# Optimization experiments

Hardware: AMD Instinct MI355X
Metric: run time of the kernel (lower is better)

Reference implementation:

```python
import jax, jax.numpy as jnp
import numpy as np

N_NODES = 100000
N_EDGES = 1600000
NFEAT = 128
NHID = 128
NS = 64
NCLASS = 16
B = 8192


def setup_inputs() -> dict:
    key = jax.random.key(0)
    ks = jax.random.split(key, 12)
    s = jax.random.normal(ks[0], (B, NS), dtype=jnp.float32)
    x = jax.random.normal(ks[1], (N_NODES, NFEAT), dtype=jnp.float32)
    row = jax.random.randint(ks[2], (N_EDGES,), 0, N_NODES)
    col = jax.random.randint(ks[3], (N_EDGES,), 0, N_NODES)
    val = jax.random.uniform(ks[4], (N_EDGES,), dtype=jnp.float32)
    index = jax.random.randint(ks[5], (B,), 0, N_NODES)
    # learned parameters (glorot-ish scale)
    W1 = jax.random.normal(ks[6], (NFEAT, NHID), dtype=jnp.float32) / np.sqrt(NFEAT)
    b1 = jnp.zeros((NHID,), dtype=jnp.float32)
    W2 = jax.random.normal(ks[7], (NHID, NHID), dtype=jnp.float32) / np.sqrt(NHID)
    b2 = jnp.zeros((NHID,), dtype=jnp.float32)
    Wl = jax.random.normal(ks[8], (NHID + NS, NCLASS), dtype=jnp.float32) / np.sqrt(NHID + NS)
    bl = jnp.zeros((NCLASS,), dtype=jnp.float32)
    return {"s": s, "x": x, "row": row, "col": col, "val": val,
            "index": index, "W1": W1, "b1": b1, "W2": W2, "b2": b2,
            "Wl": Wl, "bl": bl}


def reference(s, x, row, col, val, index, W1, b1, W2, b2, Wl, bl):
    n = x.shape[0]

    def spmm(h):
        # adj @ h with adj in COO form: out[r] += val_e * h[c]
        return jax.ops.segment_sum(val[:, None] * h[col], row, num_segments=n)

    # dropout is identity in eval mode (training=False)
    h = jax.nn.relu(spmm(x @ W1) + b1)          # gc1 + relu
    h = spmm(h @ W2) + b2                        # gc2
    z = jnp.concatenate([h[index], s], axis=1) @ Wl + bl  # [B, nclass]
    return jax.nn.log_softmax(z, axis=1)
```

## Files before the change

### kernel.cpp

```cpp
#include <hip/hip_runtime.h>
#include <hip/hip_fp16.h>
#include <math.h>

#define N_NODES 100000
#define N_EDGES 1600000
#define NFEAT 128
#define NHID 128
#define NS 64
#define NCLASS 16
#define BB 8192

#define B1_SHIFT 11
#define NB1 49
#define SUB_SHIFT 5
#define NSUB 3125
#define CHUNKA 2048
#define HWG 256
#define BINC_CAP 2048

#define NSLICE 8
#define SLICEF 16

typedef unsigned long long ull;
typedef unsigned int uint;


__device__ __forceinline__ unsigned short f2bf(float f) {
  unsigned int u = __float_as_uint(f);
  return (unsigned short)((u + 0x7fffu + ((u >> 16) & 1u)) >> 16);
}
__device__ __forceinline__ unsigned int packbf2(float lo, float hi) {
  return (unsigned int)f2bf(lo) | ((unsigned int)f2bf(hi) << 16);
}


__device__ __forceinline__ __half2 h2zero() {
  return __builtin_bit_cast(__half2, 0u);
}
__device__ __forceinline__ __half2 h2shfl_add(__half2 a, int m) {
  int t = __shfl_xor(__builtin_bit_cast(int, a), m);
  return __hadd2(a, __builtin_bit_cast(__half2, t));
}
__device__ __forceinline__ uint relu2(uint u) {
  uint mm = ((u >> 15) & 0x10001u) * 0xFFFFu;
  return u & ~mm;
}
union U4H { uint4 u4; __half2 h[4]; };

__device__ __forceinline__ void fma_row_h(__half2* acc, __half2 v, uint4 u) {
  U4H q; q.u4 = u;
#pragma unroll
  for (int k = 0; k < 4; ++k) acc[k] = __hfma2(v, q.h[k], acc[k]);
}
__device__ __forceinline__ __half2 edge_vh2(uint e) {
  uint hb = e >> 17;
  return __builtin_bit_cast(__half2, hb * 0x10001u);
}


__device__ __forceinline__ ull pack_edge(float v, int r, int c) {
  return ((ull)(__float_as_uint(v) >> 2) << 34) | ((ull)(unsigned)r << 17) | (unsigned)c;
}
__device__ __forceinline__ int edge_col(ull p) { return (int)(p & 0x1FFFFu); }
__device__ __forceinline__ int edge_row(ull p) { return (int)((unsigned)(p >> 17) & 0x1FFFFu); }
__device__ __forceinline__ float edge_val(ull p) {
  return __uint_as_float(((unsigned)(p >> 34)) << 2);
}
__device__ __forceinline__ uint pack4(ull p) {
  uint hb = (uint)__half_as_ushort(__float2half(edge_val(p)));
  return (uint)edge_col(p) | (hb << 17);
}
__device__ __forceinline__ int keep_test(const uint* keep, int r) {
  return (keep[r >> 5] >> (r & 31)) & 1u;
}


__global__ __launch_bounds__(256) void selbuild_kernel(const int* __restrict__ index,
                                                       int* __restrict__ sel,
                                                       uint* __restrict__ keep) {
  int t = blockIdx.x * 256 + threadIdx.x;
  int r = index[t];
  sel[r] = 1;
  atomicOr(&keep[r >> 5], 1u << (r & 31));
}

__global__ __launch_bounds__(256) void selflag_kernel(const int* __restrict__ row,
                                                      const int* __restrict__ col,
                                                      const int* __restrict__ sel,
                                                      uint* __restrict__ keep) {
  int i = blockIdx.x * blockDim.x + threadIdx.x;
  int stride = gridDim.x * blockDim.x;
  for (; i < N_EDGES; i += stride)
    if (sel[row[i]]) {
      int c = col[i];
      atomicOr(&keep[c >> 5], 1u << (c & 31));
    }
}


__global__ __launch_bounds__(256) void rowlist_kernel(const uint* __restrict__ keep,
                                                      int* __restrict__ rowlist,
                                                      int* __restrict__ nkept) {
  int w = blockIdx.x * 256 + threadIdx.x;
  if (w >= NSUB) return;
  uint b = keep[w];
  int c = __popc(b);
  if (!c) return;
  int base = atomicAdd(nkept, c);
  int r0 = w << 5;
  while (b) {
    int i = __ffs(b) - 1;
    rowlist[base++] = r0 + i;
    b &= b - 1;
  }
}


__global__ __launch_bounds__(256) void histsub_kernel(const int* __restrict__ row,
                                                      const uint* __restrict__ keep,
                                                      int* __restrict__ subcnt) {
  __shared__ int lh[NSUB];
  int tid = threadIdx.x;
  for (int i = tid; i < NSUB; i += 256) lh[i] = 0;
  __syncthreads();
  for (long i = (long)blockIdx.x * 256 + tid; i < N_EDGES; i += (long)HWG * 256) {
    int r = row[i];
    if (keep_test(keep, r)) atomicAdd(&lh[r >> SUB_SHIFT], 1);
  }
  __syncthreads();
  for (int i = tid; i < NSUB; i += 256) {
    int c = lh[i];
    if (c) atomicAdd(&subcnt[i], c);
  }
}


__global__ __launch_bounds__(1024) void scanall_kernel(const int* __restrict__ subcnt,
                                                       int* __restrict__ sub_offs,
                                                       int* __restrict__ gcur1,
                                                       int* __restrict__ gcur2) {
  __shared__ int sd[1024];
  int tid = threadIdx.x;
  int b0 = tid * 4;
  int vv[4];
  int loc = 0;
#pragma unroll
  for (int k = 0; k < 4; ++k) {
    int i = b0 + k;
    vv[k] = (i < NSUB) ? subcnt[i] : 0;
    loc += vv[k];
  }
  sd[tid] = loc;
  __syncthreads();
  for (int o = 1; o < 1024; o <<= 1) {
    int add = (tid >= o) ? sd[tid - o] : 0;
    __syncthreads();
    sd[tid] += add;
    __syncthreads();
  }
  int pre = sd[tid] - loc;
#pragma unroll
  for (int k = 0; k < 4; ++k) {
    int i = b0 + k;
    if (i < NSUB) {
      sub_offs[i] = pre;
      gcur2[i] = pre;
      if ((i & 63) == 0) gcur1[i >> 6] = pre;
      pre += vv[k];
    }
  }
  if (tid == 1023) sub_offs[NSUB] = sd[1023];
}


__global__ __launch_bounds__(256) void binA_kernel(const int* __restrict__ row,
                                                   const int* __restrict__ col,
                                                   const float* __restrict__ val,
                                                   const uint* __restrict__ keep,
                                                   int* __restrict__ gcur1,
                                                   ull* __restrict__ ebuf1) {
  __shared__ ull stage[CHUNKA];
  __shared__ short bkt[CHUNKA];
  __shared__ int hist[NB1], lofs[NB1 + 1], lcur[NB1], gbase[NB1];
  int tid = threadIdx.x;
  for (long base = (long)blockIdx.x * CHUNKA; base < N_EDGES; base += (long)gridDim.x * CHUNKA) {
    int cnt = (int)min((long)CHUNKA, (long)N_EDGES - base);
    if (tid < NB1) hist[tid] = 0;
    __syncthreads();
    ull e[8]; int bk[8];
#pragma unroll
    for (int v = 0; v < 8; ++v) {
      int i = v * 256 + tid;
      bk[v] = -1;
      if (i < cnt) {
        long g = base + i;
        int r = row[g];
        if (keep_test(keep, r)) {
          e[v] = pack_edge(val[g], r, col[g]);
          bk[v] = r >> B1_SHIFT;
          atomicAdd(&hist[bk[v]], 1);
        }
      }
    }
    __syncthreads();
    if (tid < 64) {
      int h = (tid < NB1) ? hist[tid] : 0;
      int x = h;
      for (int o = 1; o < 64; o <<= 1) {
        int y = __shfl_up(x, o);
        if (tid >= o) x += y;
      }
      if (tid < NB1) { lofs[tid] = x - h; lcur[tid] = x - h; }
      if (tid == 63) lofs[NB1] = x;
    }
    __syncthreads();
#pragma unroll
    for (int v = 0; v < 8; ++v) {
      if (bk[v] >= 0) {
        int pos = atomicAdd(&lcur[bk[v]], 1);
        stage[pos] = e[v];
        bkt[pos] = (short)bk[v];
      }
    }
    __syncthreads();
    if (tid < NB1) {
      int h = hist[tid];
      if (h > 0) gbase[tid] = atomicAdd(&gcur1[tid], h);
    }
    __syncthreads();
    int tot = lofs[NB1];
    for (int s = tid; s < tot; s += 256) {
      int lo = bkt[s];
      ebuf1[gbase[lo] + (s - lofs[lo])] = stage[s];
    }
    __syncthreads();
  }
}


__global__ __launch_bounds__(256) void binB_kernel(const ull* __restrict__ ebuf1,
                                                   const int* __restrict__ sub_offs,
                                                   int* __restrict__ gcur2,
                                                   ull* __restrict__ edat8) {
  __shared__ ull stage[CHUNKA];
  __shared__ short bkt[CHUNKA];
  __shared__ int hist[64], lofs[65], lcur[64], gbase[64];
  int tid = threadIdx.x;
  int b1 = blockIdx.x >> 3, w = blockIdx.x & 7;
  int rbeg = sub_offs[b1 << 6];
  int rend = sub_offs[min((b1 + 1) << 6, NSUB)];
  for (int base = rbeg + w * CHUNKA; base < rend; base += 8 * CHUNKA) {
    int cnt = min(CHUNKA, rend - base);
    if (tid < 64) hist[tid] = 0;
    __syncthreads();
    ull e[8]; int bk[8];
#pragma unroll
    for (int v = 0; v < 8; ++v) {
      int i = v * 256 + tid;
      bk[v] = -1;
      if (i < cnt) {
        e[v] = ebuf1[base + i];
        bk[v] = (edge_row(e[v]) >> SUB_SHIFT) - (b1 << 6);
        atomicAdd(&hist[bk[v]], 1);
      }
    }
    __syncthreads();
    if (tid < 64) {
      int h = hist[tid];
      int x = h;
      for (int o = 1; o < 64; o <<= 1) {
        int y = __shfl_up(x, o);
        if (tid >= o) x += y;
      }
      lofs[tid] = x - h;
      lcur[tid] = x - h;
      if (tid == 63) lofs[64] = x;
    }
    __syncthreads();
#pragma unroll
    for (int v = 0; v < 8; ++v) {
      if (bk[v] >= 0) {
        int pos = atomicAdd(&lcur[bk[v]], 1);
        stage[pos] = e[v];
        bkt[pos] = (short)bk[v];
      }
    }
    __syncthreads();
    if (tid < 64) {
      int h = hist[tid];
      if (h > 0) gbase[tid] = atomicAdd(&gcur2[(b1 << 6) + tid], h);
    }
    __syncthreads();
    for (int s = tid; s < cnt; s += 256) {
      int lo = bkt[s];
      edat8[gbase[lo] + (s - lofs[lo])] = stage[s];
    }
    __syncthreads();
  }
}


__global__ __launch_bounds__(256) void binC_kernel(const int* __restrict__ sub_offs,
                                                   const ull* __restrict__ edat8,
                                                   ull* __restrict__ ebuf1,
                                                   uint* __restrict__ edat4,
                                                   int* __restrict__ offs) {
  __shared__ ull es[BINC_CAP];
  __shared__ int rcnt[32], rcur[32];
  int s = blockIdx.x, tid = threadIdx.x;
  int r0 = s << SUB_SHIFT;
  int beg = sub_offs[s], end = sub_offs[s + 1];
  int n = end - beg;
  if (tid < 32) rcnt[tid] = 0;
  __syncthreads();
  if (n <= BINC_CAP) {
    for (int i = tid; i < n; i += 256) {
      ull p = edat8[beg + i];
      es[i] = p;
      atomicAdd(&rcnt[edge_row(p) & 31], 1);
    }
    __syncthreads();
    if (tid < 32) {
      int h = rcnt[tid];
      int x = h;
      for (int o = 1; o < 32; o <<= 1) {
        int y = __shfl_up(x, o, 32);
        if (tid >= o) x += y;
      }
      rcur[tid] = x - h;
      offs[r0 + tid] = beg + x - h;
      if (s == NSUB - 1 && tid == 31) offs[N_NODES] = end;
    }
    __syncthreads();
    for (int i = tid; i < n; i += 256) {
      ull p = es[i];
      int pos = atomicAdd(&rcur[edge_row(p) & 31], 1);
      edat4[beg + pos] = pack4(p);
    }
  } else {
    for (int i = tid; i < n; i += 256) {
      ull p = edat8[beg + i];
      ebuf1[beg + i] = p;
      atomicAdd(&rcnt[edge_row(p) & 31], 1);
    }
    __syncthreads();
    if (tid < 32) {
      int h = rcnt[tid];
      int x = h;
      for (int o = 1; o < 32; o <<= 1) {
        int y = __shfl_up(x, o, 32);
        if (tid >= o) x += y;
      }
      rcur[tid] = x - h;
      offs[r0 + tid] = beg + x - h;
      if (s == NSUB - 1 && tid == 31) offs[N_NODES] = end;
    }
    __syncthreads();
    for (int i = tid; i < n; i += 256) {
      ull p = ebuf1[beg + i];
      int pos = atomicAdd(&rcur[edge_row(p) & 31], 1);
      edat4[beg + pos] = pack4(p);
    }
  }
}


typedef __attribute__((ext_vector_type(8))) __bf16 bf16x8;
typedef __attribute__((ext_vector_type(4))) float f32x4;
union FragU { uint4 u; bf16x8 b; };

#define LDSTR 68

__global__ __launch_bounds__(256) void gemm1_kernel(const float* __restrict__ A,
                                                    const float* __restrict__ W,
                                                    unsigned short* __restrict__ C,
                                                    int nrows) {
  __shared__ uint As_s[64 * LDSTR];
  __shared__ uint Wt_s[128 * LDSTR];
  int tid = threadIdx.x;
  int rbase = blockIdx.x * 64;

  {
    int n = tid & 127, hh = tid >> 7;
#pragma unroll
    for (int kk = 0; kk < 32; ++kk) {
      int kc = hh * 32 + kk;
      Wt_s[n * LDSTR + kc] = packbf2(W[(2 * kc) * 128 + n], W[(2 * kc + 1) * 128 + n]);
    }
  }
  {
    const float4* src = (const float4*)(A + (long)rbase * 128);
#pragma unroll
    for (int i = 0; i < 8; ++i) {
      int f = i * 256 + tid;
      int m = f >> 5;
      float4 v = (rbase + m < nrows) ? src[f] : make_float4(0.f, 0.f, 0.f, 0.f);
      int c = (f & 31) * 2;
      As_s[m * LDSTR + c]     = packbf2(v.x, v.y);
      As_s[m * LDSTR + c + 1] = packbf2(v.z, v.w);
    }
  }
  __syncthreads();

  int w = tid >> 6, lane = tid & 63;
  int quad = lane >> 4, lr = lane & 15;
  int n0 = w * 32;

  f32x4 acc[4][2];
#pragma unroll
  for (int mt = 0; mt < 4; ++mt)
#pragma unroll
    for (int nt = 0; nt < 2; ++nt) acc[mt][nt] = (f32x4){0.f, 0.f, 0.f, 0.f};

#pragma unroll
  for (int kk = 0; kk < 4; ++kk) {
    int kc = kk * 16 + quad * 4;
    FragU fb0, fb1;
    fb0.u = *(const uint4*)&Wt_s[(n0 + lr) * LDSTR + kc];
    fb1.u = *(const uint4*)&Wt_s[(n0 + 16 + lr) * LDSTR + kc];
#pragma unroll
    for (int mt = 0; mt < 4; ++mt) {
      FragU fa;
      fa.u = *(const uint4*)&As_s[(mt * 16 + lr) * LDSTR + kc];
      acc[mt][0] = __builtin_amdgcn_mfma_f32_16x16x32_bf16(fa.b, fb0.b, acc[mt][0], 0, 0, 0);
      acc[mt][1] = __builtin_amdgcn_mfma_f32_16x16x32_bf16(fa.b, fb1.b, acc[mt][1], 0, 0, 0);
    }
  }

#pragma unroll
  for (int mt = 0; mt < 4; ++mt) {
#pragma unroll
    for (int nt = 0; nt < 2; ++nt) {
      __half* cs = (__half*)(C + (size_t)(w * 2 + nt) * (N_NODES * SLICEF));
#pragma unroll
      for (int r = 0; r < 4; ++r) {
        int row = rbase + mt * 16 + quad * 4 + r;
        if (row < nrows) cs[(size_t)row * SLICEF + lr] = __float2half(acc[mt][nt][r]);
      }
    }
  }
}


__global__ __launch_bounds__(256) void gemm2f_kernel(const float* __restrict__ g2,
                                                     const float* __restrict__ W2,
                                                     const float* __restrict__ b2,
                                                     const float* __restrict__ s_in,
                                                     const float* __restrict__ Wl,
                                                     const float* __restrict__ bl,
                                                     float* __restrict__ out) {
  __shared__ uint smem[13056];
  uint* Wt_s = smem;
  uint* As_s = smem + 128 * LDSTR;
  float* ts  = (float*)smem;
  float* Wls = (float*)(smem + 128 * LDSTR);
  int tid = threadIdx.x;
  int rbase = blockIdx.x * 64;

  {
    int n = tid & 127, hh = tid >> 7;
#pragma unroll
    for (int kk = 0; kk < 32; ++kk) {
      int kc = hh * 32 + kk;
      Wt_s[n * LDSTR + kc] = packbf2(W2[(2 * kc) * 128 + n], W2[(2 * kc + 1) * 128 + n]);
    }
  }
  {
    const float4* src = (const float4*)(g2 + (long)rbase * 128);
#pragma unroll
    for (int i = 0; i < 8; ++i) {
      int f = i * 256 + tid;
      int m = f >> 5, c = (f & 31) * 2;
      float4 v = src[f];
      As_s[m * LDSTR + c]     = packbf2(v.x, v.y);
      As_s[m * LDSTR + c + 1] = packbf2(v.z, v.w);
    }
  }
  __syncthreads();

  int w = tid >> 6, lane = tid & 63;
  int quad = lane >> 4, lr = lane & 15;
  int n0 = w * 32;

  f32x4 acc[4][2];
#pragma unroll
  for (int mt = 0; mt < 4; ++mt)
#pragma unroll
    for (int nt = 0; nt < 2; ++nt) acc[mt][nt] = (f32x4){0.f, 0.f, 0.f, 0.f};

#pragma unroll
  for (int kk = 0; kk < 4; ++kk) {
    int kc = kk * 16 + quad * 4;
    FragU fb0, fb1;
    fb0.u = *(const uint4*)&Wt_s[(n0 + lr) * LDSTR + kc];
    fb1.u = *(const uint4*)&Wt_s[(n0 + 16 + lr) * LDSTR + kc];
#pragma unroll
    for (int mt = 0; mt < 4; ++mt) {
      FragU fa;
      fa.u = *(const uint4*)&As_s[(mt * 16 + lr) * LDSTR + kc];
      acc[mt][0] = __builtin_amdgcn_mfma_f32_16x16x32_bf16(fa.b, fb0.b, acc[mt][0], 0, 0, 0);
      acc[mt][1] = __builtin_amdgcn_mfma_f32_16x16x32_bf16(fa.b, fb1.b, acc[mt][1], 0, 0, 0);
    }
  }
  __syncthreads();

#pragma unroll
  for (int mt = 0; mt < 4; ++mt) {
#pragma unroll
    for (int nt = 0; nt < 2; ++nt) {
      int col = n0 + nt * 16 + lr;
      float bv = b2[col];
#pragma unroll
      for (int r = 0; r < 4; ++r)
        ts[(mt * 16 + quad * 4 + r) * 129 + col] = acc[mt][nt][r] + bv;
    }
  }
  for (int i = tid; i < 192 * 16; i += 256) Wls[i] = Wl[i];
  __syncthreads();

  int q = lane & 3;
  int mrow = w * 16 + (lane >> 2);
  int b = rbase + mrow;
  float z[16];
#pragma unroll
  for (int c = 0; c < 16; ++c) z[c] = 0.f;
  int k0 = q * 48;
  for (int kk = 0; kk < 48; ++kk) {
    int k = k0 + kk;
    float xv = (k < 128) ? ts[mrow * 129 + k] : s_in[(long)b * 64 + (k - 128)];
    const float* wp = Wls + k * 16;
#pragma unroll
    for (int c = 0; c < 16; ++c) z[c] = fmaf(xv, wp[c], z[c]);
  }
#pragma unroll
  for (int c = 0; c < 16; ++c) {
    z[c] += __shfl_xor(z[c], 1);
    z[c] += __shfl_xor(z[c], 2);
  }
  if (q == 0) {
#pragma unroll
    for (int c = 0; c < 16; ++c) z[c] += bl[c];
    float mx = z[0];
#pragma unroll
    for (int c = 1; c < 16; ++c) mx = fmaxf(mx, z[c]);
    float sum = 0.f;
#pragma unroll
    for (int c = 0; c < 16; ++c) sum += expf(z[c] - mx);
    float lse = mx + logf(sum);
    float4* ob = (float4*)(out + (long)b * 16);
    ob[0] = make_float4(z[0] - lse, z[1] - lse, z[2] - lse, z[3] - lse);
    ob[1] = make_float4(z[4] - lse, z[5] - lse, z[6] - lse, z[7] - lse);
    ob[2] = make_float4(z[8] - lse, z[9] - lse, z[10] - lse, z[11] - lse);
    ob[3] = make_float4(z[12] - lse, z[13] - lse, z[14] - lse, z[15] - lse);
  }
}


__global__ __launch_bounds__(256) void spmm_row_kernel(const int* __restrict__ offs,
                                                       const uint* __restrict__ edat4,
                                                       const unsigned short* __restrict__ a,
                                                       const float* __restrict__ bias,
                                                       unsigned short* __restrict__ h1,
                                                       const int* __restrict__ rowlist,
                                                       const int* __restrict__ nkept) {
  int nk = *nkept;
  int rblk = blockIdx.x >> 3;
  if (rblk * 32 >= nk) return;
  int s = blockIdx.x & 7;
  int tid = threadIdx.x, lane = tid & 63;
  int li = rblk * 32 + (tid >> 3);
  int g = (lane >> 1) & 3, h = lane & 1, h8 = h * 8;
  const unsigned short* as = a + (size_t)s * (N_NODES * SLICEF);
  bool active = li < nk;
  int r = 0, j = 0, jend = 0;
  if (active) {
    r = __builtin_nontemporal_load(&rowlist[li]);
    j = __builtin_nontemporal_load(&offs[r]) + g;
    jend = __builtin_nontemporal_load(&offs[r + 1]);
  }
  __half2 acc[4] = {h2zero(), h2zero(), h2zero(), h2zero()};
  for (; j + 4 < jend; j += 8) {
    uint e0 = __builtin_nontemporal_load(&edat4[j]);
    uint e1 = __builtin_nontemporal_load(&edat4[j + 4]);
    uint4 u0 = *(const uint4*)(as + (size_t)(e0 & 0x1FFFFu) * SLICEF + h8);
    uint4 u1 = *(const uint4*)(as + (size_t)(e1 & 0x1FFFFu) * SLICEF + h8);
    fma_row_h(acc, edge_vh2(e0), u0);
    fma_row_h(acc, edge_vh2(e1), u1);
  }
  if (j < jend) {
    uint e = __builtin_nontemporal_load(&edat4[j]);
    uint4 u = *(const uint4*)(as + (size_t)(e & 0x1FFFFu) * SLICEF + h8);
    fma_row_h(acc, edge_vh2(e), u);
  }
#pragma unroll
  for (int k = 0; k < 4; ++k) {
    acc[k] = h2shfl_add(acc[k], 2);
    acc[k] = h2shfl_add(acc[k], 4);
  }
  if (active && (lane & 6) == 0) {
    const float* bp = bias + s * SLICEF + h8;
    float4 b0 = *(const float4*)bp;
    float4 b1v = *(const float4*)(bp + 4);
    uint4 o;
    o.x = relu2(__builtin_bit_cast(uint, __hadd2(acc[0], __floats2half2_rn(b0.x, b0.y))));
    o.y = relu2(__builtin_bit_cast(uint, __hadd2(acc[1], __floats2half2_rn(b0.z, b0.w))));
    o.z = relu2(__builtin_bit_cast(uint, __hadd2(acc[2], __floats2half2_rn(b1v.x, b1v.y))));
    o.w = relu2(__builtin_bit_cast(uint, __hadd2(acc[3], __floats2half2_rn(b1v.z, b1v.w))));
    *(uint4*)(h1 + (size_t)s * (N_NODES * SLICEF) + (size_t)r * SLICEF + h8) = o;
  }
}

__global__ __launch_bounds__(256) void spmm_sel_kernel(const int* __restrict__ offs,
                                                       const uint* __restrict__ edat4,
                                                       const unsigned short* __restrict__ h1,
                                                       const int* __restrict__ index,
                                                       float* __restrict__ g2) {
  int s = blockIdx.x & 7;
  int bblk = blockIdx.x >> 3;
  int tid = threadIdx.x, lane = tid & 63;
  int b = bblk * 32 + (tid >> 3);
  int g = (lane >> 1) & 3, h = lane & 1, h8 = h * 8;
  const unsigned short* hs = h1 + (size_t)s * (N_NODES * SLICEF);
  int r = __builtin_nontemporal_load(&index[b]);
  int j = __builtin_nontemporal_load(&offs[r]) + g;
  int jend = __builtin_nontemporal_load(&offs[r + 1]);
  __half2 acc[4] = {h2zero(), h2zero(), h2zero(), h2zero()};
  for (; j + 4 < jend; j += 8) {
    uint e0 = __builtin_nontemporal_load(&edat4[j]);
    uint e1 = __builtin_nontemporal_load(&edat4[j + 4]);
    uint4 u0 = *(const uint4*)(hs + (size_t)(e0 & 0x1FFFFu) * SLICEF + h8);
    uint4 u1 = *(const uint4*)(hs + (size_t)(e1 & 0x1FFFFu) * SLICEF + h8);
    fma_row_h(acc, edge_vh2(e0), u0);
    fma_row_h(acc, edge_vh2(e1), u1);
  }
  if (j < jend) {
    uint e = __builtin_nontemporal_load(&edat4[j]);
    uint4 u = *(const uint4*)(hs + (size_t)(e & 0x1FFFFu) * SLICEF + h8);
    fma_row_h(acc, edge_vh2(e), u);
  }
#pragma unroll
  for (int k = 0; k < 4; ++k) {
    acc[k] = h2shfl_add(acc[k], 2);
    acc[k] = h2shfl_add(acc[k], 4);
  }
  if ((lane & 6) == 0) {
    float* op = g2 + (size_t)b * 128 + s * SLICEF + h8;
    *(float4*)op = make_float4(__low2float(acc[0]), __high2float(acc[0]),
                               __low2float(acc[1]), __high2float(acc[1]));
    *(float4*)(op + 4) = make_float4(__low2float(acc[2]), __high2float(acc[2]),
                                     __low2float(acc[3]), __high2float(acc[3]));
  }
}


extern "C" void kernel_launch(void* const* d_in, const int* in_sizes, int n_in,
                              void* d_out, int out_size, void* d_ws, size_t ws_size,
                              hipStream_t stream) {
  const float* s_in  = (const float*)d_in[0];
  const float* x     = (const float*)d_in[1];
  const int*   row   = (const int*)d_in[2];
  const int*   col   = (const int*)d_in[3];
  const float* val   = (const float*)d_in[4];
  const int*   index = (const int*)d_in[5];
  const float* W1    = (const float*)d_in[6];
  const float* b1    = (const float*)d_in[7];
  const float* W2    = (const float*)d_in[8];
  const float* b2    = (const float*)d_in[9];
  const float* Wl    = (const float*)d_in[10];
  const float* bl    = (const float*)d_in[11];
  float* out = (float*)d_out;

  ull* edat8 = (ull*)d_ws;
  ull* ebuf1 = edat8 + N_EDGES;
  uint* edat4 = (uint*)ebuf1;
  unsigned short* a  = (unsigned short*)(ebuf1 + N_EDGES);
  unsigned short* h1 = a + (size_t)N_NODES * 128;
  float* g2   = (float*)(h1 + (size_t)N_NODES * 128);
  int* sel    = (int*)(g2 + (size_t)BB * 128);
  int* rowlist = sel;
  int* subcnt = sel + N_NODES;
  uint* keep  = (uint*)(subcnt + NSUB);
  int* offs   = (int*)(keep + NSUB);
  int* sub_offs = offs + (N_NODES + 1);
  int* gcur1  = sub_offs + (NSUB + 1);
  int* gcur2  = gcur1 + NB1;
  int* nkept  = gcur2 + NSUB;

  hipMemsetAsync(sel, 0, (N_NODES + 2 * NSUB) * sizeof(int), stream);
  hipMemsetAsync(nkept, 0, sizeof(int), stream);

  selbuild_kernel<<<BB / 256, 256, 0, stream>>>(index, sel, keep);
  selflag_kernel<<<4096, 256, 0, stream>>>(row, col, sel, keep);
  histsub_kernel<<<HWG, 256, 0, stream>>>(row, keep, subcnt);
  scanall_kernel<<<1, 1024, 0, stream>>>(subcnt, sub_offs, gcur1, gcur2);
  rowlist_kernel<<<(NSUB + 255) / 256, 256, 0, stream>>>(keep, rowlist, nkept);

  binA_kernel<<<512, 256, 0, stream>>>(row, col, val, keep, gcur1, ebuf1);
  binB_kernel<<<NB1 * 8, 256, 0, stream>>>(ebuf1, sub_offs, gcur2, edat8);
  binC_kernel<<<NSUB, 256, 0, stream>>>(sub_offs, edat8, ebuf1, edat4, offs);

  gemm1_kernel<<<(N_NODES + 63) / 64, 256, 0, stream>>>(x, W1, a, N_NODES);
  spmm_row_kernel<<<NSUB * NSLICE, 256, 0, stream>>>(offs, edat4, a, b1, h1, rowlist, nkept);
  spmm_sel_kernel<<<(BB / 32) * NSLICE, 256, 0, stream>>>(offs, edat4, h1, index, g2);
  gemm2f_kernel<<<BB / 64, 256, 0, stream>>>(g2, W2, b2, s_in, Wl, bl, out);
}
```

Baseline: 357.9 us.

## Switch feature matrices from sliced layout to row-major with wave-per-row SpMM

Replaces the 8-slice column-partitioned layout of the intermediate feature matrices with plain row-major 128-wide rows. Each SpMM wave now handles one whole row (16 lanes by 8 features, 4 edge groups) and skips rows by testing the keep bitmap directly. This removes the rowlist compaction kernel and its memset, and the repeated per-slice reads of edge data. gemm1 now processes two 64-row tiles per block so the W1 staging is shared. The cost is launching a block for every node, including rows that are not kept, and reading edge lists through a single wave per row.

```diff
diff --git a/kernel.cpp b/kernel.cpp
--- a/kernel.cpp
+++ b/kernel.cpp
@@ -17,9 +17,6 @@
 #define CHUNKA 2048
 #define HWG 256
 #define BINC_CAP 2048
-
-#define NSLICE 8
-#define SLICEF 16
 
 typedef unsigned long long ull;
 typedef unsigned int uint;
@@ -95,24 +92,6 @@
       int c = col[i];
       atomicOr(&keep[c >> 5], 1u << (c & 31));
     }
-}
-
-
-__global__ __launch_bounds__(256) void rowlist_kernel(const uint* __restrict__ keep,
-                                                      int* __restrict__ rowlist,
-                                                      int* __restrict__ nkept) {
-  int w = blockIdx.x * 256 + threadIdx.x;
-  if (w >= NSUB) return;
-  uint b = keep[w];
-  int c = __popc(b);
-  if (!c) return;
-  int base = atomicAdd(nkept, c);
-  int r0 = w << 5;
-  while (b) {
-    int i = __ffs(b) - 1;
-    rowlist[base++] = r0 + i;
-    b &= b - 1;
-  }
 }
 
 
@@ -378,7 +357,6 @@
   __shared__ uint As_s[64 * LDSTR];
   __shared__ uint Wt_s[128 * LDSTR];
   int tid = threadIdx.x;
-  int rbase = blockIdx.x * 64;
 
   {
     int n = tid & 127, hh = tid >> 7;
@@ -388,54 +366,61 @@
       Wt_s[n * LDSTR + kc] = packbf2(W[(2 * kc) * 128 + n], W[(2 * kc + 1) * 128 + n]);
     }
   }
-  {
-    const float4* src = (const float4*)(A + (long)rbase * 128);
-#pragma unroll
-    for (int i = 0; i < 8; ++i) {
-      int f = i * 256 + tid;
-      int m = f >> 5;
-      float4 v = (rbase + m < nrows) ? src[f] : make_float4(0.f, 0.f, 0.f, 0.f);
-      int c = (f & 31) * 2;
-      As_s[m * LDSTR + c]     = packbf2(v.x, v.y);
-      As_s[m * LDSTR + c + 1] = packbf2(v.z, v.w);
-    }
-  }
-  __syncthreads();
 
   int w = tid >> 6, lane = tid & 63;
   int quad = lane >> 4, lr = lane & 15;
   int n0 = w * 32;
 
-  f32x4 acc[4][2];
-#pragma unroll
-  for (int mt = 0; mt < 4; ++mt)
-#pragma unroll
-    for (int nt = 0; nt < 2; ++nt) acc[mt][nt] = (f32x4){0.f, 0.f, 0.f, 0.f};
-
-#pragma unroll
-  for (int kk = 0; kk < 4; ++kk) {
-    int kc = kk * 16 + quad * 4;
-    FragU fb0, fb1;
-    fb0.u = *(const uint4*)&Wt_s[(n0 + lr) * LDSTR + kc];
-    fb1.u = *(const uint4*)&Wt_s[(n0 + 16 + lr) * LDSTR + kc];
+#pragma unroll
+  for (int t = 0; t < 2; ++t) {
+    int rbase = blockIdx.x * 128 + t * 64;
+    __syncthreads();
+    {
+      const float4* src = (const float4*)(A + (long)rbase * 128);
+#pragma unroll
+      for (int i = 0; i < 8; ++i) {
+        int f = i * 256 + tid;
+        int m = f >> 5;
+        float4 v = (rbase + m < nrows) ? src[f] : make_float4(0.f, 0.f, 0.f, 0.f);
+        int c = (f & 31) * 2;
+        As_s[m * LDSTR + c]     = packbf2(v.x, v.y);
+        As_s[m * LDSTR + c + 1] = packbf2(v.z, v.w);
+      }
+    }
+    __syncthreads();
+
+    f32x4 acc[4][2];
+#pragma unroll
+    for (int mt = 0; mt < 4; ++mt)
+#pragma unroll
+      for (int nt = 0; nt < 2; ++nt) acc[mt][nt] = (f32x4){0.f, 0.f, 0.f, 0.f};
+
+#pragma unroll
+    for (int kk = 0; kk < 4; ++kk) {
+      int kc = kk * 16 + quad * 4;
+      FragU fb0, fb1;
+      fb0.u = *(const uint4*)&Wt_s[(n0 + lr) * LDSTR + kc];
+      fb1.u = *(const uint4*)&Wt_s[(n0 + 16 + lr) * LDSTR + kc];
+#pragma unroll
+      for (int mt = 0; mt < 4; ++mt) {
+        FragU fa;
+        fa.u = *(const uint4*)&As_s[(mt * 16 + lr) * LDSTR + kc];
+        acc[mt][0] = __builtin_amdgcn_mfma_f32_16x16x32_bf16(fa.b, fb0.b, acc[mt][0], 0, 0, 0);
+        acc[mt][1] = __builtin_amdgcn_mfma_f32_16x16x32_bf16(fa.b, fb1.b, acc[mt][1], 0, 0, 0);
+      }
+    }
+
+    __half* cs = (__half*)C;
 #pragma unroll
     for (int mt = 0; mt < 4; ++mt) {
-      FragU fa;
-      fa.u = *(const uint4*)&As_s[(mt * 16 + lr) * LDSTR + kc];
-      acc[mt][0] = __builtin_amdgcn_mfma_f32_16x16x32_bf16(fa.b, fb0.b, acc[mt][0], 0, 0, 0);
-      acc[mt][1] = __builtin_amdgcn_mfma_f32_16x16x32_bf16(fa.b, fb1.b, acc[mt][1], 0, 0, 0);
-    }
-  }
-
-#pragma unroll
-  for (int mt = 0; mt < 4; ++mt) {
-#pragma unroll
-    for (int nt = 0; nt < 2; ++nt) {
-      __half* cs = (__half*)(C + (size_t)(w * 2 + nt) * (N_NODES * SLICEF));
-#pragma unroll
-      for (int r = 0; r < 4; ++r) {
-        int row = rbase + mt * 16 + quad * 4 + r;
-        if (row < nrows) cs[(size_t)row * SLICEF + lr] = __float2half(acc[mt][nt][r]);
+#pragma unroll
+      for (int nt = 0; nt < 2; ++nt) {
+        int col = n0 + nt * 16 + lr;
+#pragma unroll
+        for (int r = 0; r < 4; ++r) {
+          int row = rbase + mt * 16 + quad * 4 + r;
+          if (row < nrows) cs[(size_t)row * 128 + col] = __float2half(acc[mt][nt][r]);
+        }
       }
     }
   }
@@ -561,44 +546,35 @@
                                                        const unsigned short* __restrict__ a,
                                                        const float* __restrict__ bias,
                                                        unsigned short* __restrict__ h1,
-                                                       const int* __restrict__ rowlist,
-                                                       const int* __restrict__ nkept) {
-  int nk = *nkept;
-  int rblk = blockIdx.x >> 3;
-  if (rblk * 32 >= nk) return;
-  int s = blockIdx.x & 7;
-  int tid = threadIdx.x, lane = tid & 63;
-  int li = rblk * 32 + (tid >> 3);
-  int g = (lane >> 1) & 3, h = lane & 1, h8 = h * 8;
-  const unsigned short* as = a + (size_t)s * (N_NODES * SLICEF);
-  bool active = li < nk;
-  int r = 0, j = 0, jend = 0;
-  if (active) {
-    r = __builtin_nontemporal_load(&rowlist[li]);
-    j = __builtin_nontemporal_load(&offs[r]) + g;
-    jend = __builtin_nontemporal_load(&offs[r + 1]);
-  }
+                                                       const uint* __restrict__ keep) {
+  int wave = threadIdx.x >> 6;
+  int lane = threadIdx.x & 63;
+  int r = blockIdx.x * 4 + wave;
+  if (!keep_test(keep, r)) return;
+  int g = lane >> 4, l = lane & 15;
+  int s = offs[r], e = offs[r + 1];
   __half2 acc[4] = {h2zero(), h2zero(), h2zero(), h2zero()};
-  for (; j + 4 < jend; j += 8) {
-    uint e0 = __builtin_nontemporal_load(&edat4[j]);
-    uint e1 = __builtin_nontemporal_load(&edat4[j + 4]);
-    uint4 u0 = *(const uint4*)(as + (size_t)(e0 & 0x1FFFFu) * SLICEF + h8);
-    uint4 u1 = *(const uint4*)(as + (size_t)(e1 & 0x1FFFFu) * SLICEF + h8);
+  int j = s + g;
+  for (; j + 4 < e; j += 8) {
+    uint e0 = edat4[j];
+    uint e1 = edat4[j + 4];
+    uint4 u0 = *(const uint4*)(a + (size_t)(e0 & 0x1FFFFu) * 128 + l * 8);
+    uint4 u1 = *(const uint4*)(a + (size_t)(e1 & 0x1FFFFu) * 128 + l * 8);
     fma_row_h(acc, edge_vh2(e0), u0);
     fma_row_h(acc, edge_vh2(e1), u1);
   }
-  if (j < jend) {
-    uint e = __builtin_nontemporal_load(&edat4[j]);
-    uint4 u = *(const uint4*)(as + (size_t)(e & 0x1FFFFu) * SLICEF + h8);
-    fma_row_h(acc, edge_vh2(e), u);
+  if (j < e) {
+    uint e0 = edat4[j];
+    uint4 u = *(const uint4*)(a + (size_t)(e0 & 0x1FFFFu) * 128 + l * 8);
+    fma_row_h(acc, edge_vh2(e0), u);
   }
 #pragma unroll
   for (int k = 0; k < 4; ++k) {
-    acc[k] = h2shfl_add(acc[k], 2);
-    acc[k] = h2shfl_add(acc[k], 4);
-  }
-  if (active && (lane & 6) == 0) {
-    const float* bp = bias + s * SLICEF + h8;
+    acc[k] = h2shfl_add(acc[k], 16);
+    acc[k] = h2shfl_add(acc[k], 32);
+  }
+  if (g == 0) {
+    const float* bp = bias + l * 8;
     float4 b0 = *(const float4*)bp;
     float4 b1v = *(const float4*)(bp + 4);
     uint4 o;
@@ -606,7 +582,7 @@
     o.y = relu2(__builtin_bit_cast(uint, __hadd2(acc[1], __floats2half2_rn(b0.z, b0.w))));
     o.z = relu2(__builtin_bit_cast(uint, __hadd2(acc[2], __floats2half2_rn(b1v.x, b1v.y))));
     o.w = relu2(__builtin_bit_cast(uint, __hadd2(acc[3], __floats2half2_rn(b1v.z, b1v.w))));
-    *(uint4*)(h1 + (size_t)s * (N_NODES * SLICEF) + (size_t)r * SLICEF + h8) = o;
+    *(uint4*)(h1 + (size_t)r * 128 + l * 8) = o;
   }
 }
 
@@ -615,36 +591,34 @@
                                                        const unsigned short* __restrict__ h1,
                                                        const int* __restrict__ index,
                                                        float* __restrict__ g2) {
-  int s = blockIdx.x & 7;
-  int bblk = blockIdx.x >> 3;
-  int tid = threadIdx.x, lane = tid & 63;
-  int b = bblk * 32 + (tid >> 3);
-  int g = (lane >> 1) & 3, h = lane & 1, h8 = h * 8;
-  const unsigned short* hs = h1 + (size_t)s * (N_NODES * SLICEF);
-  int r = __builtin_nontemporal_load(&index[b]);
-  int j = __builtin_nontemporal_load(&offs[r]) + g;
-  int jend = __builtin_nontemporal_load(&offs[r + 1]);
+  int wave = threadIdx.x >> 6;
+  int lane = threadIdx.x & 63;
+  int b = blockIdx.x * 4 + wave;
+  int g = lane >> 4, l = lane & 15;
+  int r = index[b];
+  int s = offs[r], e = offs[r + 1];
   __half2 acc[4] = {h2zero(), h2zero(), h2zero(), h2zero()};
-  for (; j + 4 < jend; j += 8) {
-    uint e0 = __builtin_nontemporal_load(&edat4[j]);
-    uint e1 = __builtin_nontemporal_load(&edat4[j + 4]);
-    uint4 u0 = *(const uint4*)(hs + (size_t)(e0 & 0x1FFFFu) * SLICEF + h8);
-    uint4 u1 = *(const uint4*)(hs + (size_t)(e1 & 0x1FFFFu) * SLICEF + h8);
+  int j = s + g;
+  for (; j + 4 < e; j += 8) {
+    uint e0 = edat4[j];
+    uint e1 = edat4[j + 4];
+    uint4 u0 = *(const uint4*)(h1 + (size_t)(e0 & 0x1FFFFu) * 128 + l * 8);
+    uint4 u1 = *(const uint4*)(h1 + (size_t)(e1 & 0x1FFFFu) * 128 + l * 8);
     fma_row_h(acc, edge_vh2(e0), u0);
     fma_row_h(acc, edge_vh2(e1), u1);
   }
-  if (j < jend) {
-    uint e = __builtin_nontemporal_load(&edat4[j]);
-    uint4 u = *(const uint4*)(hs + (size_t)(e & 0x1FFFFu) * SLICEF + h8);
-    fma_row_h(acc, edge_vh2(e), u);
+  if (j < e) {
+    uint e0 = edat4[j];
+    uint4 u = *(const uint4*)(h1 + (size_t)(e0 & 0x1FFFFu) * 128 + l * 8);
+    fma_row_h(acc, edge_vh2(e0), u);
   }
 #pragma unroll
   for (int k = 0; k < 4; ++k) {
-    acc[k] = h2shfl_add(acc[k], 2);
-    acc[k] = h2shfl_add(acc[k], 4);
-  }
-  if ((lane & 6) == 0) {
-    float* op = g2 + (size_t)b * 128 + s * SLICEF + h8;
+    acc[k] = h2shfl_add(acc[k], 16);
+    acc[k] = h2shfl_add(acc[k], 32);
+  }
+  if (g == 0) {
+    float* op = g2 + (size_t)b * 128 + l * 8;
     *(float4*)op = make_float4(__low2float(acc[0]), __high2float(acc[0]),
                                __low2float(acc[1]), __high2float(acc[1]));
     *(float4*)(op + 4) = make_float4(__low2float(acc[2]), __high2float(acc[2]),
@@ -677,30 +651,26 @@
   unsigned short* h1 = a + (size_t)N_NODES * 128;
   float* g2   = (float*)(h1 + (size_t)N_NODES * 128);
   int* sel    = (int*)(g2 + (size_t)BB * 128);
-  int* rowlist = sel;
   int* subcnt = sel + N_NODES;
   uint* keep  = (uint*)(subcnt + NSUB);
   int* offs   = (int*)(keep + NSUB);
   int* sub_offs = offs + (N_NODES + 1);
   int* gcur1  = sub_offs + (NSUB + 1);
   int* gcur2  = gcur1 + NB1;
-  int* nkept  = gcur2 + NSUB;
 
   hipMemsetAsync(sel, 0, (N_NODES + 2 * NSUB) * sizeof(int), stream);
-  hipMemsetAsync(nkept, 0, sizeof(int), stream);
 
   selbuild_kernel<<<BB / 256, 256, 0, stream>>>(index, sel, keep);
   selflag_kernel<<<4096, 256, 0, stream>>>(row, col, sel, keep);
   histsub_kernel<<<HWG, 256, 0, stream>>>(row, keep, subcnt);
   scanall_kernel<<<1, 1024, 0, stream>>>(subcnt, sub_offs, gcur1, gcur2);
-  rowlist_kernel<<<(NSUB + 255) / 256, 256, 0, stream>>>(keep, rowlist, nkept);
 
   binA_kernel<<<512, 256, 0, stream>>>(row, col, val, keep, gcur1, ebuf1);
   binB_kernel<<<NB1 * 8, 256, 0, stream>>>(ebuf1, sub_offs, gcur2, edat8);
   binC_kernel<<<NSUB, 256, 0, stream>>>(sub_offs, edat8, ebuf1, edat4, offs);
 
-  gemm1_kernel<<<(N_NODES + 63) / 64, 256, 0, stream>>>(x, W1, a, N_NODES);
-  spmm_row_kernel<<<NSUB * NSLICE, 256, 0, stream>>>(offs, edat4, a, b1, h1, rowlist, nkept);
-  spmm_sel_kernel<<<(BB / 32) * NSLICE, 256, 0, stream>>>(offs, edat4, h1, index, g2);
+  gemm1_kernel<<<(N_NODES + 127) / 128, 256, 0, stream>>>(x, W1, a, N_NODES);
+  spmm_row_kernel<<<N_NODES / 4, 256, 0, stream>>>(offs, edat4, a, b1, h1, keep);
+  spmm_sel_kernel<<<BB / 4, 256, 0, stream>>>(offs, edat4, h1, index, g2);
   gemm2f_kernel<<<BB / 64, 256, 0, stream>>>(g2, W2, b2, s_in, Wl, bl, out);
 }
```

Result: faster. 296.0 us (-17.3%).
